# Performance work log

Hardware: AMD Instinct MI355X
Metric: run time of the kernel (lower is better)

## Reference

```python
import jax, jax.numpy as jnp
import numpy as np

N, E = 50000, 800000
IN_D, HID, H1, OUT_D, H2, EDGE_D = 64, 16, 8, 64, 2, 1
NEG_SLOPE = 0.2


def gatv2_layer(x, src, dst, edge_attr, Wl, Wr, We, att, bias, concat):
    """PyG GATv2Conv (add_self_loops=False, share_weights=False), eval mode (no dropout)."""
    n = x.shape[0]
    H, C = att.shape
    xl = (x @ Wl).reshape(n, H, C)            # source transform
    xr = (x @ Wr).reshape(n, H, C)            # target transform
    ee = (edge_attr @ We).reshape(-1, H, C)   # edge embedding
    z = jax.nn.leaky_relu(xl[src] + xr[dst] + ee, NEG_SLOPE)  # [E,H,C]
    score = jnp.einsum('ehc,hc->eh', z, att)                  # [E,H]
    # softmax over incoming edges per target node
    m = jax.ops.segment_max(score, dst, num_segments=n)
    m = jnp.where(jnp.isfinite(m), m, 0.0)
    a = jnp.exp(score - m[dst])
    denom = jax.ops.segment_sum(a, dst, num_segments=n)
    alpha = a / (denom[dst] + 1e-16)                          # [E,H]
    msg = xl[src] * alpha[..., None]                          # [E,H,C]
    out = jax.ops.segment_sum(msg, dst, num_segments=n)       # [N,H,C]
    if concat:
        return out.reshape(n, H * C) + bias
    return out.mean(axis=1) + bias


def layer_norm(x, g, b):
    mu = x.mean(-1, keepdims=True)
    var = ((x - mu) ** 2).mean(-1, keepdims=True)
    return (x - mu) * jax.lax.rsqrt(var + 1e-5) * g + b


def setup_inputs() -> dict:
    key = jax.random.key(0)
    ks = jax.random.split(key, 24)
    def w(k, *shape):
        fan_in = shape[0]
        return jax.random.normal(k, shape, dtype=jnp.float32) * (1.0 / np.sqrt(fan_in))
    inp = {
        'x': jax.random.normal(ks[0], (N, IN_D), dtype=jnp.float32),
        'edge_index': jax.random.randint(ks[1], (2, E), 0, N, dtype=jnp.int64),
        'edge_attr': jax.random.normal(ks[2], (E, EDGE_D), dtype=jnp.float32),
        # layer 1 (heads=8, out=16, concat)
        'w1_l': w(ks[3], IN_D, H1 * HID), 'w1_r': w(ks[4], IN_D, H1 * HID),
        'w1_e': w(ks[5], EDGE_D, H1 * HID),
        'att1': jax.random.normal(ks[6], (H1, HID), dtype=jnp.float32) * 0.1,
        'b1': jnp.zeros((H1 * HID,), dtype=jnp.float32),
        # layer 2 (heads=2, out=64, mean)
        'w2_l': w(ks[7], H1 * HID, H2 * OUT_D), 'w2_r': w(ks[8], H1 * HID, H2 * OUT_D),
        'w2_e': w(ks[9], EDGE_D, H2 * OUT_D),
        'att2': jax.random.normal(ks[10], (H2, OUT_D), dtype=jnp.float32) * 0.1,
        'b2': jnp.zeros((OUT_D,), dtype=jnp.float32),
        # classifier: Linear + LayerNorm + GELU + ResidualBlockv2
        'wc': w(ks[11], OUT_D, OUT_D), 'bc': jnp.zeros((OUT_D,), dtype=jnp.float32),
        'ln_g': jnp.ones((OUT_D,), dtype=jnp.float32), 'ln_b': jnp.zeros((OUT_D,), dtype=jnp.float32),
        'wr': w(ks[12], OUT_D, OUT_D), 'br': jnp.zeros((OUT_D,), dtype=jnp.float32),
        'lnr_g': jnp.ones((OUT_D,), dtype=jnp.float32), 'lnr_b': jnp.zeros((OUT_D,), dtype=jnp.float32),
    }
    return inp


def reference(x, edge_index, edge_attr, w1_l, w1_r, w1_e, att1, b1,
              w2_l, w2_r, w2_e, att2, b2, wc, bc, ln_g, ln_b, wr, br, lnr_g, lnr_b):
    src, dst = edge_index[0], edge_index[1]
    h = jax.nn.relu(gatv2_layer(x, src, dst, edge_attr, w1_l, w1_r, w1_e, att1, b1, True))
    h = jax.nn.relu(gatv2_layer(h, src, dst, edge_attr, w2_l, w2_r, w2_e, att2, b2, False))
    h = jax.nn.gelu(layer_norm(h @ wc + bc, ln_g, ln_b), approximate=False)
    # ResidualBlockv2: Linear -> LayerNorm -> GELU with residual skip
    h = h + jax.nn.gelu(layer_norm(h @ wr + br, lnr_g, lnr_b), approximate=False)
    return h
```

## Files before the change

### kernel.cpp

```cpp
#include <hip/hip_runtime.h>
#include <math.h>

#define NNODE 50000
#define NEDGE 800000
#define NBLK_SCAN 196

__device__ __forceinline__ float wsum64(float v) {
    #pragma unroll
    for (int m = 32; m >= 1; m >>= 1) v += __shfl_xor(v, m, 64);
    return v;
}

__device__ __forceinline__ float gelu_exact(float x) {
    return 0.5f * x * (1.0f + erff(x * 0.70710678118654752f));
}

__device__ __forceinline__ float lrelu(float z) { return z > 0.f ? z : 0.2f * z; }

__global__ void fill_u32(unsigned* __restrict__ p, unsigned v, int n) {
    int i = blockIdx.x * blockDim.x + threadIdx.x;
    if (i < n) p[i] = v;
}

__global__ __launch_bounds__(256) void build_deg(const int* __restrict__ ei, int* __restrict__ deg) {
    int e = blockIdx.x * 256 + threadIdx.x;
    if (e >= NEDGE) return;
    atomicAdd(&deg[ei[NEDGE + e]], 1);
}

__global__ __launch_bounds__(256) void scan1(const int* __restrict__ deg,
                                             int* __restrict__ partial,
                                             int* __restrict__ bsum) {
    __shared__ int tmp[256];
    int t = threadIdx.x;
    int gid = blockIdx.x * 256 + t;
    int v = (gid < NNODE) ? deg[gid] : 0;
    tmp[t] = v;
    __syncthreads();
    #pragma unroll
    for (int off = 1; off < 256; off <<= 1) {
        int u = (t >= off) ? tmp[t - off] : 0;
        __syncthreads();
        tmp[t] += u;
        __syncthreads();
    }
    if (gid < NNODE) partial[gid] = tmp[t] - v;
    if (t == 255) bsum[blockIdx.x] = tmp[255];
}

__global__ __launch_bounds__(256) void scan2(int* __restrict__ bsum, int* __restrict__ boff) {
    __shared__ int tmp[256];
    int t = threadIdx.x;
    int v = (t < NBLK_SCAN) ? bsum[t] : 0;
    tmp[t] = v;
    __syncthreads();
    #pragma unroll
    for (int off = 1; off < 256; off <<= 1) {
        int u = (t >= off) ? tmp[t - off] : 0;
        __syncthreads();
        tmp[t] += u;
        __syncthreads();
    }
    if (t < NBLK_SCAN) boff[t] = tmp[t] - v;
}

__global__ __launch_bounds__(256) void scan3(const int* __restrict__ partial,
                                             const int* __restrict__ boff,
                                             int* __restrict__ base,
                                             int* __restrict__ cursor) {
    int gid = blockIdx.x * 256 + threadIdx.x;
    if (gid < NNODE) {
        int b = partial[gid] + boff[blockIdx.x];
        base[gid] = b;
        cursor[gid] = b;
    }
    if (gid == 0) base[NNODE] = NEDGE;
}

__global__ __launch_bounds__(256) void scatter_edges(const int* __restrict__ ei,
                                                     const float* __restrict__ ea,
                                                     int* __restrict__ cursor,
                                                     int2* __restrict__ se) {
    int e = blockIdx.x * 256 + threadIdx.x;
    if (e >= NEDGE) return;
    int d = ei[NEDGE + e];
    int i = atomicAdd(&cursor[d], 1);
    se[i] = make_int2(ei[e], __float_as_int(ea[e]));
}

__global__ __launch_bounds__(256) void node_xform1(const float* __restrict__ x,
                                                   const float* __restrict__ wl,
                                                   const float* __restrict__ wr,
                                                   float* __restrict__ xl,
                                                   float* __restrict__ xr) {
    __shared__ float xrow[8][64];
    int t = threadIdx.x;
    int n0 = blockIdx.x * 8;
    for (int k = t; k < 8 * 64; k += 256) xrow[k >> 6][k & 63] = x[(size_t)n0 * 64 + k];
    __syncthreads();
    const float* w;
    float* o;
    int c;
    if (t < 128) { w = wl; c = t; o = xl; }
    else         { w = wr; c = t - 128; o = xr; }
    float acc[8] = {0.f, 0.f, 0.f, 0.f, 0.f, 0.f, 0.f, 0.f};
    for (int i = 0; i < 64; ++i) {
        float wv = w[i * 128 + c];
        #pragma unroll
        for (int k = 0; k < 8; ++k) acc[k] += xrow[k][i] * wv;
    }
    #pragma unroll
    for (int k = 0; k < 8; ++k) o[(size_t)(n0 + k) * 128 + c] = acc[k];
}

__global__ __launch_bounds__(256) void node_xform2(const float* __restrict__ h1,
                                                   const float* __restrict__ wl,
                                                   const float* __restrict__ wr,
                                                   float* __restrict__ xl,
                                                   float* __restrict__ xr) {
    __shared__ float hrow[8][128];
    int t = threadIdx.x;
    int n0 = blockIdx.x * 8;
    for (int k = t; k < 8 * 128; k += 256) hrow[k >> 7][k & 127] = h1[(size_t)n0 * 128 + k];
    __syncthreads();
    const float* w;
    float* o;
    int c;
    if (t < 128) { w = wl; c = t; o = xl; }
    else         { w = wr; c = t - 128; o = xr; }
    float acc[8] = {0.f, 0.f, 0.f, 0.f, 0.f, 0.f, 0.f, 0.f};
    for (int i = 0; i < 128; ++i) {
        float wv = w[i * 128 + c];
        #pragma unroll
        for (int k = 0; k < 8; ++k) acc[k] += hrow[k][i] * wv;
    }
    #pragma unroll
    for (int k = 0; k < 8; ++k) o[(size_t)(n0 + k) * 128 + c] = acc[k];
}

__global__ __launch_bounds__(256) void fused1(const int* __restrict__ base,
                                              const int2* __restrict__ se,
                                              const float* __restrict__ xl,
                                              const float* __restrict__ xr,
                                              const float* __restrict__ w1e,
                                              const float* __restrict__ att1,
                                              const float* __restrict__ b1,
                                              float* __restrict__ h1) {
    int t = threadIdx.x;
    int wv = t >> 6, ln = t & 63;
    int n = blockIdx.x * 4 + wv;
    int ch = 2 * ln;
    float xr0 = xr[(size_t)n * 128 + ch], xr1 = xr[(size_t)n * 128 + ch + 1];
    float we0 = w1e[ch], we1 = w1e[ch + 1];
    float at0 = att1[ch], at1 = att1[ch + 1];
    int i0 = base[n], i1 = base[n + 1];
    float m = -INFINITY, den = 0.f, o0 = 0.f, o1 = 0.f;
    if (i0 < i1) {
        int2 r = se[i0];
        float x0 = xl[(size_t)r.x * 128 + ch];
        float x1 = xl[(size_t)r.x * 128 + ch + 1];
        float a = __int_as_float(r.y);
        for (int i = i0 + 1; i < i1; ++i) {
            int2 rn = se[i];
            float nx0 = xl[(size_t)rn.x * 128 + ch];
            float nx1 = xl[(size_t)rn.x * 128 + ch + 1];
            float na = __int_as_float(rn.y);
            float part = lrelu(x0 + xr0 + a * we0) * at0 + lrelu(x1 + xr1 + a * we1) * at1;
            part += __shfl_xor(part, 1, 64);
            part += __shfl_xor(part, 2, 64);
            part += __shfl_xor(part, 4, 64);
            float mn = fmaxf(m, part);
            float sc = __expf(m - mn);
            float p  = __expf(part - mn);
            den = den * sc + p;
            o0  = o0 * sc + p * x0;
            o1  = o1 * sc + p * x1;
            m = mn;
            x0 = nx0; x1 = nx1; a = na;
        }
        float part = lrelu(x0 + xr0 + a * we0) * at0 + lrelu(x1 + xr1 + a * we1) * at1;
        part += __shfl_xor(part, 1, 64);
        part += __shfl_xor(part, 2, 64);
        part += __shfl_xor(part, 4, 64);
        float mn = fmaxf(m, part);
        float sc = __expf(m - mn);
        float p  = __expf(part - mn);
        den = den * sc + p;
        o0  = o0 * sc + p * x0;
        o1  = o1 * sc + p * x1;
    }
    float inv = 1.f / (den + 1e-16f);
    float v0 = o0 * inv + b1[ch];
    float v1 = o1 * inv + b1[ch + 1];
    h1[(size_t)n * 128 + ch]     = v0 > 0.f ? v0 : 0.f;
    h1[(size_t)n * 128 + ch + 1] = v1 > 0.f ? v1 : 0.f;
}

__global__ __launch_bounds__(256) void fused2(const int* __restrict__ base,
                                              const int2* __restrict__ se,
                                              const float* __restrict__ xl,
                                              const float* __restrict__ xr,
                                              const float* __restrict__ w2e,
                                              const float* __restrict__ att2,
                                              const float* __restrict__ b2,
                                              float* __restrict__ h2) {
    int t = threadIdx.x;
    int wv = t >> 6, ln = t & 63;
    int n = blockIdx.x * 4 + wv;
    int ch = 2 * ln;
    float xr0 = xr[(size_t)n * 128 + ch], xr1 = xr[(size_t)n * 128 + ch + 1];
    float we0 = w2e[ch], we1 = w2e[ch + 1];
    float at0 = att2[ch], at1 = att2[ch + 1];
    int i0 = base[n], i1 = base[n + 1];
    float m = -INFINITY, den = 0.f, o0 = 0.f, o1 = 0.f;
    if (i0 < i1) {
        int2 r = se[i0];
        float x0 = xl[(size_t)r.x * 128 + ch];
        float x1 = xl[(size_t)r.x * 128 + ch + 1];
        float a = __int_as_float(r.y);
        for (int i = i0 + 1; i < i1; ++i) {
            int2 rn = se[i];
            float nx0 = xl[(size_t)rn.x * 128 + ch];
            float nx1 = xl[(size_t)rn.x * 128 + ch + 1];
            float na = __int_as_float(rn.y);
            float part = lrelu(x0 + xr0 + a * we0) * at0 + lrelu(x1 + xr1 + a * we1) * at1;
            part += __shfl_xor(part, 1, 64);
            part += __shfl_xor(part, 2, 64);
            part += __shfl_xor(part, 4, 64);
            part += __shfl_xor(part, 8, 64);
            part += __shfl_xor(part, 16, 64);
            float mn = fmaxf(m, part);
            float sc = __expf(m - mn);
            float p  = __expf(part - mn);
            den = den * sc + p;
            o0  = o0 * sc + p * x0;
            o1  = o1 * sc + p * x1;
            m = mn;
            x0 = nx0; x1 = nx1; a = na;
        }
        float part = lrelu(x0 + xr0 + a * we0) * at0 + lrelu(x1 + xr1 + a * we1) * at1;
        part += __shfl_xor(part, 1, 64);
        part += __shfl_xor(part, 2, 64);
        part += __shfl_xor(part, 4, 64);
        part += __shfl_xor(part, 8, 64);
        part += __shfl_xor(part, 16, 64);
        float mn = fmaxf(m, part);
        float sc = __expf(m - mn);
        float p  = __expf(part - mn);
        den = den * sc + p;
        o0  = o0 * sc + p * x0;
        o1  = o1 * sc + p * x1;
    }
    float inv = 1.f / (den + 1e-16f);
    float v0 = o0 * inv, v1 = o1 * inv;
    float u0 = __shfl_xor(v0, 32, 64);
    float u1 = __shfl_xor(v1, 32, 64);
    if (ln < 32) {
        int c = 2 * ln;
        float r0 = 0.5f * (v0 + u0) + b2[c];
        float r1 = 0.5f * (v1 + u1) + b2[c + 1];
        h2[(size_t)n * 64 + c]     = r0 > 0.f ? r0 : 0.f;
        h2[(size_t)n * 64 + c + 1] = r1 > 0.f ? r1 : 0.f;
    }
}

__global__ __launch_bounds__(256) void classifier(const float* __restrict__ h2,
                                                  const float* __restrict__ wc,
                                                  const float* __restrict__ bc,
                                                  const float* __restrict__ lng,
                                                  const float* __restrict__ lnb,
                                                  const float* __restrict__ wr,
                                                  const float* __restrict__ br,
                                                  const float* __restrict__ lrg,
                                                  const float* __restrict__ lrb,
                                                  float* __restrict__ out) {
    __shared__ float rowA[4][64];
    __shared__ float rowB[4][64];
    int t = threadIdx.x;
    int wv = t >> 6, ln = t & 63;
    int n = blockIdx.x * 4 + wv;
    rowA[wv][ln] = h2[(size_t)n * 64 + ln];
    __syncthreads();
    float acc = bc[ln];
    #pragma unroll 8
    for (int i = 0; i < 64; ++i) acc += rowA[wv][i] * wc[i * 64 + ln];
    float mu = wsum64(acc) * (1.f / 64.f);
    float dv = acc - mu;
    float var = wsum64(dv * dv) * (1.f / 64.f);
    float y = dv * rsqrtf(var + 1e-5f) * lng[ln] + lnb[ln];
    float g1 = gelu_exact(y);
    rowB[wv][ln] = g1;
    __syncthreads();
    float acc2 = br[ln];
    #pragma unroll 8
    for (int i = 0; i < 64; ++i) acc2 += rowB[wv][i] * wr[i * 64 + ln];
    float mu2 = wsum64(acc2) * (1.f / 64.f);
    float dv2 = acc2 - mu2;
    float var2 = wsum64(dv2 * dv2) * (1.f / 64.f);
    float y2 = dv2 * rsqrtf(var2 + 1e-5f) * lrg[ln] + lrb[ln];
    float g2 = gelu_exact(y2);
    out[(size_t)n * 64 + ln] = g1 + g2;
}

extern "C" void kernel_launch(void* const* d_in, const int* in_sizes, int n_in,
                              void* d_out, int out_size, void* d_ws, size_t ws_size,
                              hipStream_t stream) {
    const float* x    = (const float*)d_in[0];
    const int*   ei   = (const int*)d_in[1];
    const float* ea   = (const float*)d_in[2];
    const float* w1l  = (const float*)d_in[3];
    const float* w1r  = (const float*)d_in[4];
    const float* w1e  = (const float*)d_in[5];
    const float* att1 = (const float*)d_in[6];
    const float* b1   = (const float*)d_in[7];
    const float* w2l  = (const float*)d_in[8];
    const float* w2r  = (const float*)d_in[9];
    const float* w2e  = (const float*)d_in[10];
    const float* att2 = (const float*)d_in[11];
    const float* b2   = (const float*)d_in[12];
    const float* wc   = (const float*)d_in[13];
    const float* bc   = (const float*)d_in[14];
    const float* lng  = (const float*)d_in[15];
    const float* lnb  = (const float*)d_in[16];
    const float* wr   = (const float*)d_in[17];
    const float* br   = (const float*)d_in[18];
    const float* lrg  = (const float*)d_in[19];
    const float* lrb  = (const float*)d_in[20];

    float* ws = (float*)d_ws;
    const size_t N128 = (size_t)NNODE * 128;
    float* xl = ws;
    float* xr = xl + N128;
    float* h1 = xr + N128;
    float* h2 = h1 + N128;
    int2*  se      = (int2*)(h2 + (size_t)NNODE * 64);
    int*   deg     = (int*)(se + NEDGE);
    int*   partial = deg + NNODE;
    int*   base    = partial + NNODE;
    int*   cursor  = base + NNODE + 1;
    int*   bsum    = cursor + NNODE;
    int*   boff    = bsum + 256;

    const int EB = NEDGE / 256;
    const int NB8 = NNODE / 8;
    const int NB4 = NNODE / 4;

    fill_u32<<<NBLK_SCAN, 256, 0, stream>>>((unsigned*)deg, 0u, NNODE);
    build_deg<<<EB, 256, 0, stream>>>(ei, deg);
    scan1<<<NBLK_SCAN, 256, 0, stream>>>(deg, partial, bsum);
    scan2<<<1, 256, 0, stream>>>(bsum, boff);
    scan3<<<NBLK_SCAN, 256, 0, stream>>>(partial, boff, base, cursor);
    scatter_edges<<<EB, 256, 0, stream>>>(ei, ea, cursor, se);

    node_xform1<<<NB8, 256, 0, stream>>>(x, w1l, w1r, xl, xr);
    fused1<<<NB4, 256, 0, stream>>>(base, se, xl, xr, w1e, att1, b1, h1);

    node_xform2<<<NB8, 256, 0, stream>>>(h1, w2l, w2r, xl, xr);
    fused2<<<NB4, 256, 0, stream>>>(base, se, xl, xr, w2e, att2, b2, h2);

    classifier<<<NB4, 256, 0, stream>>>(h2, wc, bc, lng, lnb, wr, br, lrg, lrb,
                                        (float*)d_out);
}
```

Measured before the change: 402.9 us.

## Split wave into two half-waves processing alternate edges with float4 gathers

Each 64-lane wave now covers a node's 128 channels with 32 lanes of float4 loads, and the two half-waves walk alternate incoming edges in parallel. Their online-softmax states are merged at the end with a cross-half shuffle. This doubles edge-level parallelism per wave, halves the serial dependency chain of exp/rescale per node, and widens gathers to 16-byte loads. In exchange it adds merge shuffles and exps, and uses -1e30 instead of -inf as the initial max.

```diff
diff --git a/kernel.cpp b/kernel.cpp
--- a/kernel.cpp
+++ b/kernel.cpp
@@ -148,52 +148,77 @@
                                               float* __restrict__ h1) {
     int t = threadIdx.x;
     int wv = t >> 6, ln = t & 63;
+    int half = ln >> 5, sub = ln & 31;
     int n = blockIdx.x * 4 + wv;
-    int ch = 2 * ln;
-    float xr0 = xr[(size_t)n * 128 + ch], xr1 = xr[(size_t)n * 128 + ch + 1];
-    float we0 = w1e[ch], we1 = w1e[ch + 1];
-    float at0 = att1[ch], at1 = att1[ch + 1];
+    int ch = sub * 4;
+    float4 xrv = *(const float4*)(xr + (size_t)n * 128 + ch);
+    float4 wev = *(const float4*)(w1e + ch);
+    float4 atv = *(const float4*)(att1 + ch);
     int i0 = base[n], i1 = base[n + 1];
-    float m = -INFINITY, den = 0.f, o0 = 0.f, o1 = 0.f;
-    if (i0 < i1) {
-        int2 r = se[i0];
-        float x0 = xl[(size_t)r.x * 128 + ch];
-        float x1 = xl[(size_t)r.x * 128 + ch + 1];
+    float m = -1e30f, den = 0.f;
+    float4 o = make_float4(0.f, 0.f, 0.f, 0.f);
+    int i = i0 + half;
+    if (i < i1) {
+        int2 r = se[i];
+        float4 xv = *(const float4*)(xl + (size_t)r.x * 128 + ch);
         float a = __int_as_float(r.y);
-        for (int i = i0 + 1; i < i1; ++i) {
+        for (i += 2; i < i1; i += 2) {
             int2 rn = se[i];
-            float nx0 = xl[(size_t)rn.x * 128 + ch];
-            float nx1 = xl[(size_t)rn.x * 128 + ch + 1];
+            float4 nxv = *(const float4*)(xl + (size_t)rn.x * 128 + ch);
             float na = __int_as_float(rn.y);
-            float part = lrelu(x0 + xr0 + a * we0) * at0 + lrelu(x1 + xr1 + a * we1) * at1;
+            float part = lrelu(fmaf(a, wev.x, xv.x + xrv.x)) * atv.x
+                       + lrelu(fmaf(a, wev.y, xv.y + xrv.y)) * atv.y
+                       + lrelu(fmaf(a, wev.z, xv.z + xrv.z)) * atv.z
+                       + lrelu(fmaf(a, wev.w, xv.w + xrv.w)) * atv.w;
             part += __shfl_xor(part, 1, 64);
             part += __shfl_xor(part, 2, 64);
-            part += __shfl_xor(part, 4, 64);
             float mn = fmaxf(m, part);
             float sc = __expf(m - mn);
             float p  = __expf(part - mn);
             den = den * sc + p;
-            o0  = o0 * sc + p * x0;
-            o1  = o1 * sc + p * x1;
+            o.x = o.x * sc + p * xv.x;
+            o.y = o.y * sc + p * xv.y;
+            o.z = o.z * sc + p * xv.z;
+            o.w = o.w * sc + p * xv.w;
             m = mn;
-            x0 = nx0; x1 = nx1; a = na;
+            xv = nxv; a = na;
         }
-        float part = lrelu(x0 + xr0 + a * we0) * at0 + lrelu(x1 + xr1 + a * we1) * at1;
+        float part = lrelu(fmaf(a, wev.x, xv.x + xrv.x)) * atv.x
+                   + lrelu(fmaf(a, wev.y, xv.y + xrv.y)) * atv.y
+                   + lrelu(fmaf(a, wev.z, xv.z + xrv.z)) * atv.z
+                   + lrelu(fmaf(a, wev.w, xv.w + xrv.w)) * atv.w;
         part += __shfl_xor(part, 1, 64);
         part += __shfl_xor(part, 2, 64);
-        part += __shfl_xor(part, 4, 64);
         float mn = fmaxf(m, part);
         float sc = __expf(m - mn);
         float p  = __expf(part - mn);
         den = den * sc + p;
-        o0  = o0 * sc + p * x0;
-        o1  = o1 * sc + p * x1;
-    }
+        o.x = o.x * sc + p * xv.x;
+        o.y = o.y * sc + p * xv.y;
+        o.z = o.z * sc + p * xv.z;
+        o.w = o.w * sc + p * xv.w;
+        m = mn;
+    }
+    float m2   = __shfl_xor(m, 32, 64);
+    float den2 = __shfl_xor(den, 32, 64);
+    float4 o2;
+    o2.x = __shfl_xor(o.x, 32, 64);
+    o2.y = __shfl_xor(o.y, 32, 64);
+    o2.z = __shfl_xor(o.z, 32, 64);
+    o2.w = __shfl_xor(o.w, 32, 64);
+    float mn = fmaxf(m, m2);
+    float s1 = __expf(m - mn), s2 = __expf(m2 - mn);
+    den = den * s1 + den2 * s2;
     float inv = 1.f / (den + 1e-16f);
-    float v0 = o0 * inv + b1[ch];
-    float v1 = o1 * inv + b1[ch + 1];
-    h1[(size_t)n * 128 + ch]     = v0 > 0.f ? v0 : 0.f;
-    h1[(size_t)n * 128 + ch + 1] = v1 > 0.f ? v1 : 0.f;
+    if (half == 0) {
+        float4 bv = *(const float4*)(b1 + ch);
+        float4 res;
+        res.x = fmaxf((o.x * s1 + o2.x * s2) * inv + bv.x, 0.f);
+        res.y = fmaxf((o.y * s1 + o2.y * s2) * inv + bv.y, 0.f);
+        res.z = fmaxf((o.z * s1 + o2.z * s2) * inv + bv.z, 0.f);
+        res.w = fmaxf((o.w * s1 + o2.w * s2) * inv + bv.w, 0.f);
+        *(float4*)(h1 + (size_t)n * 128 + ch) = res;
+    }
 }
 
 __global__ __launch_bounds__(256) void fused2(const int* __restrict__ base,
@@ -206,61 +231,90 @@
                                               float* __restrict__ h2) {
     int t = threadIdx.x;
     int wv = t >> 6, ln = t & 63;
+    int half = ln >> 5, sub = ln & 31;
     int n = blockIdx.x * 4 + wv;
-    int ch = 2 * ln;
-    float xr0 = xr[(size_t)n * 128 + ch], xr1 = xr[(size_t)n * 128 + ch + 1];
-    float we0 = w2e[ch], we1 = w2e[ch + 1];
-    float at0 = att2[ch], at1 = att2[ch + 1];
+    int ch = sub * 4;
+    float4 xrv = *(const float4*)(xr + (size_t)n * 128 + ch);
+    float4 wev = *(const float4*)(w2e + ch);
+    float4 atv = *(const float4*)(att2 + ch);
     int i0 = base[n], i1 = base[n + 1];
-    float m = -INFINITY, den = 0.f, o0 = 0.f, o1 = 0.f;
-    if (i0 < i1) {
-        int2 r = se[i0];
-        float x0 = xl[(size_t)r.x * 128 + ch];
-        float x1 = xl[(size_t)r.x * 128 + ch + 1];
+    float m = -1e30f, den = 0.f;
+    float4 o = make_float4(0.f, 0.f, 0.f, 0.f);
+    int i = i0 + half;
+    if (i < i1) {
+        int2 r = se[i];
+        float4 xv = *(const float4*)(xl + (size_t)r.x * 128 + ch);
         float a = __int_as_float(r.y);
-        for (int i = i0 + 1; i < i1; ++i) {
+        for (i += 2; i < i1; i += 2) {
             int2 rn = se[i];
-            float nx0 = xl[(size_t)rn.x * 128 + ch];
-            float nx1 = xl[(size_t)rn.x * 128 + ch + 1];
+            float4 nxv = *(const float4*)(xl + (size_t)rn.x * 128 + ch);
             float na = __int_as_float(rn.y);
-            float part = lrelu(x0 + xr0 + a * we0) * at0 + lrelu(x1 + xr1 + a * we1) * at1;
+            float part = lrelu(fmaf(a, wev.x, xv.x + xrv.x)) * atv.x
+                       + lrelu(fmaf(a, wev.y, xv.y + xrv.y)) * atv.y
+                       + lrelu(fmaf(a, wev.z, xv.z + xrv.z)) * atv.z
+                       + lrelu(fmaf(a, wev.w, xv.w + xrv.w)) * atv.w;
             part += __shfl_xor(part, 1, 64);
             part += __shfl_xor(part, 2, 64);
             part += __shfl_xor(part, 4, 64);
             part += __shfl_xor(part, 8, 64);
-            part += __shfl_xor(part, 16, 64);
             float mn = fmaxf(m, part);
             float sc = __expf(m - mn);
             float p  = __expf(part - mn);
             den = den * sc + p;
-            o0  = o0 * sc + p * x0;
-            o1  = o1 * sc + p * x1;
+            o.x = o.x * sc + p * xv.x;
+            o.y = o.y * sc + p * xv.y;
+            o.z = o.z * sc + p * xv.z;
+            o.w = o.w * sc + p * xv.w;
             m = mn;
-            x0 = nx0; x1 = nx1; a = na;
+            xv = nxv; a = na;
         }
-        float part = lrelu(x0 + xr0 + a * we0) * at0 + lrelu(x1 + xr1 + a * we1) * at1;
+        float part = lrelu(fmaf(a, wev.x, xv.x + xrv.x)) * atv.x
+                   + lrelu(fmaf(a, wev.y, xv.y + xrv.y)) * atv.y
+                   + lrelu(fmaf(a, wev.z, xv.z + xrv.z)) * atv.z
+                   + lrelu(fmaf(a, wev.w, xv.w + xrv.w)) * atv.w;
         part += __shfl_xor(part, 1, 64);
         part += __shfl_xor(part, 2, 64);
         part += __shfl_xor(part, 4, 64);
         part += __shfl_xor(part, 8, 64);
-        part += __shfl_xor(part, 16, 64);
         float mn = fmaxf(m, part);
         float sc = __expf(m - mn);
         float p  = __expf(part - mn);
         den = den * sc + p;
-        o0  = o0 * sc + p * x0;
-        o1  = o1 * sc + p * x1;
-    }
+        o.x = o.x * sc + p * xv.x;
+        o.y = o.y * sc + p * xv.y;
+        o.z = o.z * sc + p * xv.z;
+        o.w = o.w * sc + p * xv.w;
+        m = mn;
+    }
+    float m2   = __shfl_xor(m, 32, 64);
+    float den2 = __shfl_xor(den, 32, 64);
+    float4 o2;
+    o2.x = __shfl_xor(o.x, 32, 64);
+    o2.y = __shfl_xor(o.y, 32, 64);
+    o2.z = __shfl_xor(o.z, 32, 64);
+    o2.w = __shfl_xor(o.w, 32, 64);
+    float mn = fmaxf(m, m2);
+    float s1 = __expf(m - mn), s2 = __expf(m2 - mn);
+    den = den * s1 + den2 * s2;
     float inv = 1.f / (den + 1e-16f);
-    float v0 = o0 * inv, v1 = o1 * inv;
-    float u0 = __shfl_xor(v0, 32, 64);
-    float u1 = __shfl_xor(v1, 32, 64);
-    if (ln < 32) {
-        int c = 2 * ln;
-        float r0 = 0.5f * (v0 + u0) + b2[c];
-        float r1 = 0.5f * (v1 + u1) + b2[c + 1];
-        h2[(size_t)n * 64 + c]     = r0 > 0.f ? r0 : 0.f;
-        h2[(size_t)n * 64 + c + 1] = r1 > 0.f ? r1 : 0.f;
+    float4 v;
+    v.x = (o.x * s1 + o2.x * s2) * inv;
+    v.y = (o.y * s1 + o2.y * s2) * inv;
+    v.z = (o.z * s1 + o2.z * s2) * inv;
+    v.w = (o.w * s1 + o2.w * s2) * inv;
+    float4 u;
+    u.x = __shfl_xor(v.x, 16, 64);
+    u.y = __shfl_xor(v.y, 16, 64);
+    u.z = __shfl_xor(v.z, 16, 64);
+    u.w = __shfl_xor(v.w, 16, 64);
+    if (half == 0 && sub < 16) {
+        float4 bv = *(const float4*)(b2 + ch);
+        float4 res;
+        res.x = fmaxf(0.5f * (v.x + u.x) + bv.x, 0.f);
+        res.y = fmaxf(0.5f * (v.y + u.y) + bv.y, 0.f);
+        res.z = fmaxf(0.5f * (v.z + u.z) + bv.z, 0.f);
+        res.w = fmaxf(0.5f * (v.w + u.w) + bv.w, 0.f);
+        *(float4*)(h2 + (size_t)n * 64 + ch) = res;
     }
 }
 
```

Result: faster. 373.3 us (-7.3%).
